# Performance work log

Measured on AMD Instinct MI355X. Metric: run time of the kernel, lower is better.

## Reference

```python
import jax, jax.numpy as jnp
import numpy as np

B, S, NH, D_IN = 64, 512, 4, 256   # batch, seq_len, rnn n_head, input_dim
H = 256                            # hidden_dim == attention activation_dim
AH = 256                           # attention_hidden_dim (attn out_dim)
OUT = 3                            # output_dim (sentiment classes)


def setup_inputs() -> dict:
    key = jax.random.key(0)
    ks = jax.random.split(key, 9)
    def p(k, shape, scale=0.05):
        return jax.random.normal(k, shape, dtype=jnp.float32) * scale
    return dict(
        x=jax.random.normal(ks[0], (B, S, NH, D_IN), dtype=jnp.float32),
        Wk=p(ks[1], (D_IN, H)), bk=jnp.zeros((H,), jnp.float32),
        Wq=p(ks[2], (H, H)),    bq=jnp.zeros((H,), jnp.float32),
        w_mlp=p(ks[3], (2 * H,)),
        Wproj=p(ks[4], (H, AH)), bproj=jnp.zeros((AH,), jnp.float32),
        W1=p(ks[5], (D_IN + AH, H)), b1=jnp.zeros((H,), jnp.float32),
        W2=p(ks[6], (H, H)),    b2=jnp.zeros((H,), jnp.float32),
        Wo=p(ks[7], (NH * H, OUT)), bo=jnp.zeros((OUT,), jnp.float32),
    )


def _cell(x_t, hidden, params):
    Wk, bk, Wq, bq, w_mlp, Wproj, bproj, W1, b1, W2, b2, Wo, bo = params
    kx = x_t @ Wk + bk           # [B, NH, H]  keys from step input
    qx = hidden @ Wq + bq        # [B, NH, H]  queries from hidden state
    w1, w2 = w_mlp[:H], w_mlp[H:]
    # MLP score: s[b,i,j] = tanh(cat(kx[b,j], qx[b,i]) . w) = tanh(kx[b,j].w1 + qx[b,i].w2)
    score = jnp.tanh((qx @ w2)[:, :, None] + (kx @ w1)[:, None, :])  # [B, NH, NH]
    score = jax.nn.softmax(score, axis=-1)
    attn = jnp.einsum('bij,bjh->bih', score, kx) @ Wproj + bproj     # [B, NH, AH]
    concat = jnp.concatenate([x_t, attn], axis=-1)                   # [B, NH, D_IN+AH]
    hidden_new = jax.nn.relu(concat @ W1 + b1) @ W2 + b2             # [B, NH, H]
    logits = hidden_new.reshape(B, NH * H) @ Wo + bo                 # [B, OUT]
    out = jax.nn.log_softmax(logits, axis=-1)
    return out, hidden_new


def reference(x, Wk, bk, Wq, bq, w_mlp, Wproj, bproj, W1, b1, W2, b2, Wo, bo):
    params = (Wk, bk, Wq, bq, w_mlp, Wproj, bproj, W1, b1, W2, b2, Wo, bo)
    h0 = jnp.zeros((B, NH, H), x.dtype)
    xs = jnp.swapaxes(x, 0, 1)  # [S, B, NH, D_IN] for scan over time
    def step(h, x_t):
        out, h_new = _cell(x_t, h, params)
        return h_new, out
    h_final, outs = jax.lax.scan(step, h0, xs)
    # return_sequence=False: last-step log-softmax output and final hidden
    return outs[-1], h_final
```

## Files before the change

### kernel.cpp

```cpp
#include <hip/hip_runtime.h>
#include <hip/hip_bf16.h>
#include <math.h>

#define BB   64
#define SS   512
#define NHH  4
#define DD   256
#define HH   256
#define LDH  264

typedef __attribute__((ext_vector_type(8))) short  short8;
typedef __attribute__((ext_vector_type(4))) float  floatx4;

#define OFF_V2     0
#define OFF_CB1    256
#define OFF_C2     512
#define OFF_CKW    513
#define OFF_QW     768
#define OFF_WK1    1024
#define OFF_BKP    1280
#define OFF_VT     1536
#define OFF_RU     1792
#define OFF_WFUSE  67328
#define OFF_WKF    132864
#define OFF_PACK   198400
#define OFF_CH     263936

__device__ __forceinline__ unsigned short f2b(float f) {
  __hip_bfloat16 h = __float2bfloat16(f);
  return __builtin_bit_cast(unsigned short, h);
}
__device__ __forceinline__ float b2f(unsigned short u) {
  unsigned v = (unsigned)u << 16;
  return __builtin_bit_cast(float, v);
}

__global__ __launch_bounds__(256) void initA_kernel(
    const float* __restrict__ Wproj, const float* __restrict__ W1,
    const float* __restrict__ bk, const float* __restrict__ bproj,
    const float* __restrict__ Wq, const float* __restrict__ w_mlp,
    float* __restrict__ ws)
{
  int tid = threadIdx.x;
  int bx = blockIdx.x;
  const float* W1b = W1 + 256 * 256;
  if (bx < 256) {
    __shared__ float row[256];
    row[tid] = Wproj[bx * 256 + tid];
    __syncthreads();
    float acc = 0.f;
#pragma unroll 8
    for (int k = 0; k < 256; ++k)
      acc = fmaf(row[k], W1b[k * 256 + tid], acc);
    ws[OFF_WFUSE + bx * 256 + tid] = acc;
  } else if (bx == 256) {
    float acc = bproj[tid];
#pragma unroll 8
    for (int k = 0; k < 256; ++k)
      acc = fmaf(bk[k], Wproj[k * 256 + tid], acc);
    ws[OFF_BKP + tid] = acc;
  } else {
    const float4* Wq4 = (const float4*)(Wq + tid * 256);
    const float4* w24 = (const float4*)(w_mlp + 256);
    float a = 0.f;
    for (int k = 0; k < 64; ++k) {
      float4 wv = Wq4[k], xv = w24[k];
      a = fmaf(wv.x, xv.x, fmaf(wv.y, xv.y, fmaf(wv.z, xv.z, fmaf(wv.w, xv.w, a))));
    }
    ws[OFF_VT + tid] = a;
  }
}

__global__ __launch_bounds__(256) void initB_kernel(
    const float* __restrict__ Wk, const float* __restrict__ W1,
    const float* __restrict__ b1, const float* __restrict__ W2,
    const float* __restrict__ b2, const float* __restrict__ bq,
    const float* __restrict__ bk, const float* __restrict__ w_mlp,
    float* __restrict__ ws)
{
  int tid = threadIdx.x;
  int bx = blockIdx.x;
  if (bx < 256) {
    __shared__ float row[256];
    row[tid] = Wk[bx * 256 + tid];
    __syncthreads();
    float acc = 0.f;
    const float* Wf = ws + OFF_WFUSE;
#pragma unroll 8
    for (int k = 0; k < 256; ++k)
      acc = fmaf(row[k], Wf[k * 256 + tid], acc);
    ws[OFF_WKF + bx * 256 + tid] = acc;
  } else if (bx == 256) {
    const float* W1b = W1 + 256 * 256;
    float acc = b1[tid];
#pragma unroll 8
    for (int k = 0; k < 256; ++k)
      acc = fmaf(ws[OFF_BKP + k], W1b[k * 256 + tid], acc);
    ws[OFF_CB1 + tid] = acc;
  } else if (bx == 257) {
    __shared__ float red[256];
    {
      const float4* W24 = (const float4*)(W2 + tid * 256);
      const float4* v4  = (const float4*)(ws + OFF_VT);
      float a = 0.f;
      for (int k = 0; k < 64; ++k) {
        float4 wv = W24[k], xv = v4[k];
        a = fmaf(wv.x, xv.x, fmaf(wv.y, xv.y, fmaf(wv.z, xv.z, fmaf(wv.w, xv.w, a))));
      }
      ws[OFF_V2 + tid] = a;
    }
    red[tid] = bq[tid] * w_mlp[256 + tid];
    __syncthreads();
    for (int s = 128; s; s >>= 1) { if (tid < s) red[tid] += red[tid + s]; __syncthreads(); }
    float s2 = red[0];
    __syncthreads();
    ws[OFF_QW + tid] = s2;
    red[tid] = b2[tid] * ws[OFF_VT + tid];
    __syncthreads();
    for (int s = 128; s; s >>= 1) { if (tid < s) red[tid] += red[tid + s]; __syncthreads(); }
    if (tid == 0) ws[OFF_C2] = red[0] + s2;
    __syncthreads();
    red[tid] = bk[tid] * w_mlp[tid];
    __syncthreads();
    for (int s = 128; s; s >>= 1) { if (tid < s) red[tid] += red[tid + s]; __syncthreads(); }
    if (tid == 0) ws[OFF_CKW] = red[0];
  } else {
    const float4* Wk4 = (const float4*)(Wk + tid * 256);
    const float4* w14 = (const float4*)(w_mlp);
    float a = 0.f;
    for (int k = 0; k < 64; ++k) {
      float4 wv = Wk4[k], xv = w14[k];
      a = fmaf(wv.x, xv.x, fmaf(wv.y, xv.y, fmaf(wv.z, xv.z, fmaf(wv.w, xv.w, a))));
    }
    ws[OFF_WK1 + tid] = a;
  }
}

__global__ __launch_bounds__(256) void initC_kernel(
    const float* __restrict__ W1, float* __restrict__ ws)
{
  int idx = blockIdx.x * 256 + threadIdx.x;
  int mat = idx >> 16;
  int rem = idx & 65535;
  int j    = rem & 7;
  int lane = (rem >> 3) & 63;
  int ks   = (rem >> 9) & 7;
  int pan  = rem >> 12;
  int k = ks * 32 + ((lane >> 4) << 3) + j;
  int n = pan * 16 + (lane & 15);
  float v = (mat == 0) ? ws[OFF_WKF + k * 256 + n] : W1[k * 256 + n];
  ((unsigned short*)(ws + OFF_PACK))[idx] = f2b(v);
}

__device__ __forceinline__ void mfma_gemm4(
    const unsigned short* A_lds, const short8* __restrict__ Bp,
    const float* __restrict__ bias, floatx4 acc[4][4], int l, int w)
{
  int col = l & 15, quad = l >> 4;
#pragma unroll
  for (int pp = 0; pp < 4; ++pp) {
    float bv = bias ? bias[(w * 4 + pp) * 16 + col] : 0.f;
#pragma unroll
    for (int mf = 0; mf < 4; ++mf)
      acc[mf][pp] = (floatx4){bv, bv, bv, bv};
  }
  const short8* Bb = Bp + (size_t)(w * 4) * 512 + l;
  short8 bb[3][4];
#pragma unroll
  for (int pp = 0; pp < 4; ++pp) bb[0][pp] = Bb[pp * 512];
#pragma unroll
  for (int pp = 0; pp < 4; ++pp) bb[1][pp] = Bb[pp * 512 + 64];
#pragma unroll
  for (int kb = 0; kb < 8; ++kb) {
    if (kb + 2 < 8) {
#pragma unroll
      for (int pp = 0; pp < 4; ++pp)
        bb[(kb + 2) % 3][pp] = Bb[pp * 512 + (kb + 2) * 64];
    }
    short8 aa[4];
#pragma unroll
    for (int mf = 0; mf < 4; ++mf)
      aa[mf] = *(const short8*)(A_lds + (mf * 16 + col) * LDH + kb * 32 + quad * 8);
#pragma unroll
    for (int mf = 0; mf < 4; ++mf)
#pragma unroll
      for (int pp = 0; pp < 4; ++pp)
        acc[mf][pp] = __builtin_amdgcn_mfma_f32_16x16x32_bf16(
            aa[mf], bb[kb % 3][pp], acc[mf][pp], 0, 0, 0);
  }
}

__device__ __forceinline__ void acc_to_global(
    unsigned short* __restrict__ dst, const floatx4 acc[4][4],
    int l, int w, int b, int tt)
{
  int col = l & 15, quad = l >> 4;
#pragma unroll
  for (int mf = 0; mf < 4; ++mf)
#pragma unroll
    for (int r = 0; r < 4; ++r) {
      int m2 = mf * 16 + quad * 4 + r;
      size_t base = (((size_t)(tt * 16 + (m2 >> 2)) * 64 + b) * 4 + (m2 & 3)) * 256;
#pragma unroll
      for (int pp = 0; pp < 4; ++pp)
        dst[base + (w * 4 + pp) * 16 + col] = f2b(acc[mf][pp][r]);
    }
}

__device__ void precompute_block(
    int px, const float* __restrict__ x, const float* __restrict__ ws,
    float* __restrict__ kw_c, unsigned short* __restrict__ xw1_c,
    unsigned short* __restrict__ kpw_c, int t0,
    float* kwbuf, unsigned short* XS)
{
  int b  = px & 63;
  int tt = px >> 6;
  int tid = threadIdx.x;
  int l = tid & 63, w = tid >> 6;

  const float4* xsrc = (const float4*)(x + (size_t)(b * SS + t0 + tt * 16) * NHH * DD);
#pragma unroll
  for (int i = 0; i < 16; ++i) {
    int f4 = i * 256 + tid;
    int r = f4 >> 6, c4 = f4 & 63;
    float4 v = xsrc[f4];
    ushort4 h;
    h.x = f2b(v.x); h.y = f2b(v.y); h.z = f2b(v.z); h.w = f2b(v.w);
    *(ushort4*)&XS[r * LDH + c4 * 4] = h;
  }
  __syncthreads();

  const short8* wp0 = (const short8*)((const unsigned short*)(ws + OFF_PACK));
  const short8* wp1 = (const short8*)((const unsigned short*)(ws + OFF_PACK) + 65536);

  {
    float part = 0.f;
    const unsigned short* trow = XS + l * LDH + w * 64;
#pragma unroll
    for (int j8 = 0; j8 < 8; ++j8) {
      short8 tv = *(const short8*)(trow + j8 * 8);
#pragma unroll
      for (int j = 0; j < 8; ++j)
        part = fmaf(b2f((unsigned short)tv[j]), ws[OFF_WK1 + w * 64 + j8 * 8 + j], part);
    }
    kwbuf[l * 4 + w] = part;
  }

  floatx4 acc[4][4];

  mfma_gemm4(XS, wp0, nullptr, acc, l, w);
  acc_to_global(kpw_c, acc, l, w, b, tt);
  __syncthreads();

  if (tid < 64) {
    float s = kwbuf[tid * 4] + kwbuf[tid * 4 + 1] + kwbuf[tid * 4 + 2] + kwbuf[tid * 4 + 3]
            + ws[OFF_CKW];
    kw_c[((size_t)(tt * 16 + (tid >> 2)) * 64 + b) * 4 + (tid & 3)] = s;
  }

  mfma_gemm4(XS, wp1, ws + OFF_CB1, acc, l, w);
  acc_to_global(xw1_c, acc, l, w, b, tt);
}

__device__ __forceinline__ float wave_reduce_sum(float x) {
#define DPPSTEP(ctrl, rmask)                                                   \
  {                                                                            \
    int _s = __builtin_amdgcn_update_dpp(0, __builtin_bit_cast(int, x),        \
                                         (ctrl), (rmask), 0xf, true);          \
    x += __builtin_bit_cast(float, _s);                                        \
  }
  DPPSTEP(0x111, 0xf)
  DPPSTEP(0x112, 0xf)
  DPPSTEP(0x114, 0xf)
  DPPSTEP(0x118, 0xf)
  DPPSTEP(0x142, 0xa)
  DPPSTEP(0x143, 0xc)
#undef DPPSTEP
  return __builtin_bit_cast(float, __builtin_amdgcn_readlane(__builtin_bit_cast(int, x), 63));
}

__device__ __forceinline__ float tanh_fast(float y) {
  float ex = __expf(2.f * y);
  return 1.f - 2.f * __builtin_amdgcn_rcpf(ex + 1.f);
}

__device__ void seq_block(
    const unsigned short* __restrict__ xw1_c, const unsigned short* __restrict__ kpw_c,
    const float* __restrict__ kw_c, float* __restrict__ ws,
    float* __restrict__ relu_u, int t0, int n)
{
  int b = blockIdx.x;
  int tid = threadIdx.x;
  int i = tid >> 6, l = tid & 63;

  float4 v2v = ((const float4*)(ws + OFF_V2))[l];
  float c2 = ws[OFF_C2];
  float qw = ws[OFF_QW + b * 4 + i];

  const ushort4* xw = (const ushort4*)xw1_c;
  const ushort4* kp = (const ushort4*)kpw_c;

  struct Slot { ushort4 x, k0, k1, k2, k3; float4 kw; };

  auto load = [&](Slot& s, int tc) {
    size_t rb_ = (size_t)(tc * 64 + b) * 4;
    s.x  = xw[(rb_ + i) * 64 + l];
    s.k0 = kp[(rb_ + 0) * 64 + l];
    s.k1 = kp[(rb_ + 1) * 64 + l];
    s.k2 = kp[(rb_ + 2) * 64 + l];
    s.k3 = kp[(rb_ + 3) * 64 + l];
    s.kw = *(const float4*)&kw_c[rb_];
  };

  auto step = [&](Slot& s, int t) {
    float e0 = tanh_fast(qw + s.kw.x);
    float e1 = tanh_fast(qw + s.kw.y);
    float e2 = tanh_fast(qw + s.kw.z);
    float e3 = tanh_fast(qw + s.kw.w);
    float q0 = __expf(e0), q1 = __expf(e1), q2 = __expf(e2), q3 = __expf(e3);
    float inv = __builtin_amdgcn_rcpf(q0 + q1 + q2 + q3);
    float4 K0 = {b2f(s.k0.x), b2f(s.k0.y), b2f(s.k0.z), b2f(s.k0.w)};
    float4 K1 = {b2f(s.k1.x), b2f(s.k1.y), b2f(s.k1.z), b2f(s.k1.w)};
    float4 K2 = {b2f(s.k2.x), b2f(s.k2.y), b2f(s.k2.z), b2f(s.k2.w)};
    float4 K3 = {b2f(s.k3.x), b2f(s.k3.y), b2f(s.k3.z), b2f(s.k3.w)};
    float4 X  = {b2f(s.x.x), b2f(s.x.y), b2f(s.x.z), b2f(s.x.w)};
    float4 a;
    a.x = fmaf(q0, K0.x, fmaf(q1, K1.x, fmaf(q2, K2.x, q3 * K3.x)));
    a.y = fmaf(q0, K0.y, fmaf(q1, K1.y, fmaf(q2, K2.y, q3 * K3.y)));
    a.z = fmaf(q0, K0.z, fmaf(q1, K1.z, fmaf(q2, K2.z, q3 * K3.z)));
    a.w = fmaf(q0, K0.w, fmaf(q1, K1.w, fmaf(q2, K2.w, q3 * K3.w)));
    float4 u;
    u.x = fmaf(a.x, inv, X.x); u.y = fmaf(a.y, inv, X.y);
    u.z = fmaf(a.z, inv, X.z); u.w = fmaf(a.w, inv, X.w);
    float4 r;
    r.x = fmaxf(u.x, 0.f); r.y = fmaxf(u.y, 0.f);
    r.z = fmaxf(u.z, 0.f); r.w = fmaxf(u.w, 0.f);
    float d = fmaf(r.x, v2v.x, fmaf(r.y, v2v.y, fmaf(r.z, v2v.z, r.w * v2v.w)));
    qw = wave_reduce_sum(d) + c2;
    if (t0 + t == SS - 1)
      *(float4*)&relu_u[(size_t)(b * 4 + i) * 256 + l * 4] = r;
  };

  Slot s0, s1, s2, s3;
  load(s0, 0); load(s1, 1); load(s2, 2); load(s3, 3);
  for (int t = 0; t < n; t += 4) {
    int nt;
    step(s0, t);     nt = t + 4; load(s0, nt < n ? nt : n - 1);
    step(s1, t + 1); nt = t + 5; load(s1, nt < n ? nt : n - 1);
    step(s2, t + 2); nt = t + 6; load(s2, nt < n ? nt : n - 1);
    step(s3, t + 3); nt = t + 7; load(s3, nt < n ? nt : n - 1);
  }
  if (l == 0) ws[OFF_QW + b * 4 + i] = qw;
}

__global__ __launch_bounds__(256, 3) void fused_kernel(
    const float* __restrict__ x,
    float* kwB, unsigned short* xw1B, unsigned short* kpwB, int t0_pre,
    const float* kwA, const unsigned short* xw1A, const unsigned short* kpwA,
    int t0_seq, int n_seq,
    float* __restrict__ ws, float* __restrict__ relu_u)
{
  __shared__ float kwbuf[256];
  __shared__ __align__(16) unsigned short XS[64 * LDH];
  if (blockIdx.x < 64) {
    if (n_seq > 0) seq_block(xw1A, kpwA, kwA, ws, relu_u, t0_seq, n_seq);
    return;
  }
  precompute_block(blockIdx.x - 64, x, ws, kwB, xw1B, kpwB, t0_pre, kwbuf, XS);
}

__global__ __launch_bounds__(256) void final_hidden_kernel(
    const float* __restrict__ relu_u, const float* __restrict__ W2,
    const float* __restrict__ b2, float* __restrict__ out)
{
  __shared__ float rs[256];
  int row = blockIdx.x;
  int tid = threadIdx.x;
  rs[tid] = relu_u[(size_t)row * 256 + tid];
  __syncthreads();
  float acc = b2[tid];
  for (int k = 0; k < 256; ++k) acc = fmaf(rs[k], W2[k * 256 + tid], acc);
  out[192 + (size_t)row * 256 + tid] = acc;
}

__global__ __launch_bounds__(256) void final_logits_kernel(
    const float* __restrict__ hf, const float* __restrict__ Wo,
    const float* __restrict__ bo, float* __restrict__ outp)
{
  __shared__ float r0[256], r1[256], r2[256];
  int b = blockIdx.x;
  int tid = threadIdx.x;
  float a0 = 0.f, a1 = 0.f, a2 = 0.f;
  for (int k = tid; k < 1024; k += 256) {
    float h = hf[(size_t)b * 1024 + k];
    a0 = fmaf(h, Wo[k * 3 + 0], a0);
    a1 = fmaf(h, Wo[k * 3 + 1], a1);
    a2 = fmaf(h, Wo[k * 3 + 2], a2);
  }
  r0[tid] = a0; r1[tid] = a1; r2[tid] = a2;
  __syncthreads();
  for (int s = 128; s; s >>= 1) {
    if (tid < s) { r0[tid] += r0[tid + s]; r1[tid] += r1[tid + s]; r2[tid] += r2[tid + s]; }
    __syncthreads();
  }
  if (tid == 0) {
    float l0 = r0[0] + bo[0], l1 = r1[0] + bo[1], l2 = r2[0] + bo[2];
    float m = fmaxf(l0, fmaxf(l1, l2));
    float lse = m + logf(expf(l0 - m) + expf(l1 - m) + expf(l2 - m));
    outp[b * 3 + 0] = l0 - lse;
    outp[b * 3 + 1] = l1 - lse;
    outp[b * 3 + 2] = l2 - lse;
  }
}

extern "C" void kernel_launch(void* const* d_in, const int* in_sizes, int n_in,
                              void* d_out, int out_size, void* d_ws, size_t ws_size,
                              hipStream_t stream)
{
  const float* x     = (const float*)d_in[0];
  const float* Wk    = (const float*)d_in[1];
  const float* bk    = (const float*)d_in[2];
  const float* Wq    = (const float*)d_in[3];
  const float* bq    = (const float*)d_in[4];
  const float* w_mlp = (const float*)d_in[5];
  const float* Wproj = (const float*)d_in[6];
  const float* bproj = (const float*)d_in[7];
  const float* W1    = (const float*)d_in[8];
  const float* b1    = (const float*)d_in[9];
  const float* W2    = (const float*)d_in[10];
  const float* b2    = (const float*)d_in[11];
  const float* Wo    = (const float*)d_in[12];
  const float* bo    = (const float*)d_in[13];
  float* out = (float*)d_out;
  float* ws  = (float*)d_ws;

  float* ru = ws + OFF_RU;
  const long per_t = 256 + 65536;

  long ws_floats = (long)(ws_size / 4);
  long avail = ws_floats - (long)OFF_CH;

  int Tc = 128;
  while (Tc > 0 && 2L * Tc * per_t > avail) Tc -= 16;
  bool pipelined = (Tc >= 16);
  if (!pipelined) {
    Tc = 128;
    while (Tc > 16 && (long)Tc * per_t > avail) Tc -= 16;
  }

  float* bufA = ws + OFF_CH;
  float* bufB = pipelined ? bufA + (size_t)Tc * per_t : bufA;

  auto kw_of  = [&](float* base) { return base; };
  auto xw_of  = [&](float* base) { return (unsigned short*)(base + (size_t)Tc * 256); };
  auto kpw_of = [&](float* base) { return (unsigned short*)(base + (size_t)Tc * 256) + (size_t)Tc * 65536; };

  initA_kernel<<<258, 256, 0, stream>>>(Wproj, W1, bk, bproj, Wq, w_mlp, ws);
  initB_kernel<<<259, 256, 0, stream>>>(Wk, W1, b1, W2, b2, bq, bk, w_mlp, ws);
  initC_kernel<<<512, 256, 0, stream>>>(W1, ws);

  int C = (SS + Tc - 1) / Tc;

  if (pipelined) {
    for (int r = 0; r <= C; ++r) {
      bool hasPre = (r < C);
      bool hasSeq = (r >= 1);
      int t0p = r * Tc;
      int np  = hasPre ? ((SS - t0p) < Tc ? (SS - t0p) : Tc) : 0;
      int t0s = (r - 1) * Tc;
      int ns  = hasSeq ? ((SS - t0s) < Tc ? (SS - t0s) : Tc) : 0;
      float* pB = ((r & 1) ? bufB : bufA);
      float* pA = (((r - 1) & 1) ? bufB : bufA);
      int grid = 64 + (hasPre ? 64 * (np / 16) : 0);
      fused_kernel<<<grid, 256, 0, stream>>>(
          x,
          kw_of(pB), xw_of(pB), kpw_of(pB), t0p,
          kw_of(pA), xw_of(pA), kpw_of(pA), t0s, ns,
          ws, ru);
    }
  } else {
    for (int c = 0; c < C; ++c) {
      int t0 = c * Tc;
      int n = (SS - t0) < Tc ? (SS - t0) : Tc;
      fused_kernel<<<64 + 64 * (n / 16), 256, 0, stream>>>(
          x,
          kw_of(bufA), xw_of(bufA), kpw_of(bufA), t0,
          kw_of(bufA), xw_of(bufA), kpw_of(bufA), 0, 0,
          ws, ru);
      fused_kernel<<<64, 256, 0, stream>>>(
          x,
          kw_of(bufA), xw_of(bufA), kpw_of(bufA), t0,
          kw_of(bufA), xw_of(bufA), kpw_of(bufA), t0, n,
          ws, ru);
    }
  }

  final_hidden_kernel<<<BB * NHH, 256, 0, stream>>>(ru, W2, b2, out);
  final_logits_kernel<<<BB, 256, 0, stream>>>(out + 192, Wo, bo, out);
}
```

Measured before the change: 434.9 us.

## Split fused pipeline into separate precompute and sequential kernels, deepen prefetch

Replaces the double-buffered fused kernel, which overlapped precompute of the next chunk with the recurrence over the current chunk, with separate pre_kernel and seq_kernel launches over chunks as large as the workspace allows (up to the whole sequence). This cuts launch count and lets each kernel be compiled and sized on its own, since seq blocks no longer carry the precompute shared memory and launch bounds. The sequential loop's software prefetch depth also grows from 4 to 8 slots. In exchange, precompute no longer overlaps the serial recurrence, and the extra slots raise register pressure.

```diff
diff --git a/kernel.cpp b/kernel.cpp
--- a/kernel.cpp
+++ b/kernel.cpp
@@ -207,14 +207,16 @@
     }
 }
 
-__device__ void precompute_block(
-    int px, const float* __restrict__ x, const float* __restrict__ ws,
+__global__ __launch_bounds__(256, 3) void pre_kernel(
+    const float* __restrict__ x, const float* __restrict__ ws,
     float* __restrict__ kw_c, unsigned short* __restrict__ xw1_c,
-    unsigned short* __restrict__ kpw_c, int t0,
-    float* kwbuf, unsigned short* XS)
-{
-  int b  = px & 63;
-  int tt = px >> 6;
+    unsigned short* __restrict__ kpw_c, int t0)
+{
+  __shared__ float kwbuf[256];
+  __shared__ __align__(16) unsigned short XS[64 * LDH];
+
+  int b  = blockIdx.x & 63;
+  int tt = blockIdx.x >> 6;
   int tid = threadIdx.x;
   int l = tid & 63, w = tid >> 6;
 
@@ -251,7 +253,6 @@
   mfma_gemm4(XS, wp0, nullptr, acc, l, w);
   acc_to_global(kpw_c, acc, l, w, b, tt);
   __syncthreads();
-
   if (tid < 64) {
     float s = kwbuf[tid * 4] + kwbuf[tid * 4 + 1] + kwbuf[tid * 4 + 2] + kwbuf[tid * 4 + 3]
             + ws[OFF_CKW];
@@ -284,7 +285,7 @@
   return 1.f - 2.f * __builtin_amdgcn_rcpf(ex + 1.f);
 }
 
-__device__ void seq_block(
+__global__ void seq_kernel(
     const unsigned short* __restrict__ xw1_c, const unsigned short* __restrict__ kpw_c,
     const float* __restrict__ kw_c, float* __restrict__ ws,
     float* __restrict__ relu_u, int t0, int n)
@@ -341,32 +342,19 @@
       *(float4*)&relu_u[(size_t)(b * 4 + i) * 256 + l * 4] = r;
   };
 
-  Slot s0, s1, s2, s3;
-  load(s0, 0); load(s1, 1); load(s2, 2); load(s3, 3);
-  for (int t = 0; t < n; t += 4) {
-    int nt;
-    step(s0, t);     nt = t + 4; load(s0, nt < n ? nt : n - 1);
-    step(s1, t + 1); nt = t + 5; load(s1, nt < n ? nt : n - 1);
-    step(s2, t + 2); nt = t + 6; load(s2, nt < n ? nt : n - 1);
-    step(s3, t + 3); nt = t + 7; load(s3, nt < n ? nt : n - 1);
+  Slot s[8];
+#pragma unroll
+  for (int j = 0; j < 8; ++j) load(s[j], j < n ? j : n - 1);
+
+  for (int t = 0; t < n; t += 8) {
+#pragma unroll
+    for (int j = 0; j < 8; ++j) {
+      step(s[j], t + j);
+      int nt = t + 8 + j;
+      load(s[j], nt < n ? nt : n - 1);
+    }
   }
   if (l == 0) ws[OFF_QW + b * 4 + i] = qw;
-}
-
-__global__ __launch_bounds__(256, 3) void fused_kernel(
-    const float* __restrict__ x,
-    float* kwB, unsigned short* xw1B, unsigned short* kpwB, int t0_pre,
-    const float* kwA, const unsigned short* xw1A, const unsigned short* kpwA,
-    int t0_seq, int n_seq,
-    float* __restrict__ ws, float* __restrict__ relu_u)
-{
-  __shared__ float kwbuf[256];
-  __shared__ __align__(16) unsigned short XS[64 * LDH];
-  if (blockIdx.x < 64) {
-    if (n_seq > 0) seq_block(xw1A, kpwA, kwA, ws, relu_u, t0_seq, n_seq);
-    return;
-  }
-  precompute_block(blockIdx.x - 64, x, ws, kwB, xw1B, kpwB, t0_pre, kwbuf, XS);
 }
 
 __global__ __launch_bounds__(256) void final_hidden_kernel(
@@ -440,59 +428,21 @@
   long ws_floats = (long)(ws_size / 4);
   long avail = ws_floats - (long)OFF_CH;
 
-  int Tc = 128;
-  while (Tc > 0 && 2L * Tc * per_t > avail) Tc -= 16;
-  bool pipelined = (Tc >= 16);
-  if (!pipelined) {
-    Tc = 128;
-    while (Tc > 16 && (long)Tc * per_t > avail) Tc -= 16;
-  }
-
-  float* bufA = ws + OFF_CH;
-  float* bufB = pipelined ? bufA + (size_t)Tc * per_t : bufA;
-
-  auto kw_of  = [&](float* base) { return base; };
-  auto xw_of  = [&](float* base) { return (unsigned short*)(base + (size_t)Tc * 256); };
-  auto kpw_of = [&](float* base) { return (unsigned short*)(base + (size_t)Tc * 256) + (size_t)Tc * 65536; };
+  int Tc = SS;
+  while (Tc > 16 && (long)Tc * per_t > avail) Tc -= 16;
+
+  float* kw_c = ws + OFF_CH;
+  unsigned short* xw1_c = (unsigned short*)(kw_c + (size_t)Tc * 256);
+  unsigned short* kpw_c = xw1_c + (size_t)Tc * 65536;
 
   initA_kernel<<<258, 256, 0, stream>>>(Wproj, W1, bk, bproj, Wq, w_mlp, ws);
   initB_kernel<<<259, 256, 0, stream>>>(Wk, W1, b1, W2, b2, bq, bk, w_mlp, ws);
   initC_kernel<<<512, 256, 0, stream>>>(W1, ws);
 
-  int C = (SS + Tc - 1) / Tc;
-
-  if (pipelined) {
-    for (int r = 0; r <= C; ++r) {
-      bool hasPre = (r < C);
-      bool hasSeq = (r >= 1);
-      int t0p = r * Tc;
-      int np  = hasPre ? ((SS - t0p) < Tc ? (SS - t0p) : Tc) : 0;
-      int t0s = (r - 1) * Tc;
-      int ns  = hasSeq ? ((SS - t0s) < Tc ? (SS - t0s) : Tc) : 0;
-      float* pB = ((r & 1) ? bufB : bufA);
-      float* pA = (((r - 1) & 1) ? bufB : bufA);
-      int grid = 64 + (hasPre ? 64 * (np / 16) : 0);
-      fused_kernel<<<grid, 256, 0, stream>>>(
-          x,
-          kw_of(pB), xw_of(pB), kpw_of(pB), t0p,
-          kw_of(pA), xw_of(pA), kpw_of(pA), t0s, ns,
-          ws, ru);
-    }
-  } else {
-    for (int c = 0; c < C; ++c) {
-      int t0 = c * Tc;
-      int n = (SS - t0) < Tc ? (SS - t0) : Tc;
-      fused_kernel<<<64 + 64 * (n / 16), 256, 0, stream>>>(
-          x,
-          kw_of(bufA), xw_of(bufA), kpw_of(bufA), t0,
-          kw_of(bufA), xw_of(bufA), kpw_of(bufA), 0, 0,
-          ws, ru);
-      fused_kernel<<<64, 256, 0, stream>>>(
-          x,
-          kw_of(bufA), xw_of(bufA), kpw_of(bufA), t0,
-          kw_of(bufA), xw_of(bufA), kpw_of(bufA), t0, n,
-          ws, ru);
-    }
+  for (int t0 = 0; t0 < SS; t0 += Tc) {
+    int n = (SS - t0) < Tc ? (SS - t0) : Tc;
+    pre_kernel<<<64 * (n / 16), 256, 0, stream>>>(x, ws, kw_c, xw1_c, kpw_c, t0);
+    seq_kernel<<<64, 256, 0, stream>>>(xw1_c, kpw_c, kw_c, ws, ru, t0, n);
   }
 
   final_hidden_kernel<<<BB * NHH, 256, 0, stream>>>(ru, W2, b2, out);
```

Result: slower. 463.0 us (+6.5%).
